# Kernel optimization log

Hardware: AMD Instinct MI355X
Metric: run time of the kernel (lower is better)

Reference implementation:

```python
import jax, jax.numpy as jnp
import numpy as np

N_NODES = 100000
N_EDGES = 1600000
NUM_FEATURES = 64
HIDDEN = 64
NUM_CLASSES = 16


def setup_inputs() -> dict:
    key = jax.random.key(0)
    ks = jax.random.split(key, 8)
    x = jax.random.normal(ks[0], (N_NODES, NUM_FEATURES), dtype=jnp.float32)
    edge_index = jax.random.randint(ks[1], (2, N_EDGES), 0, N_NODES, dtype=jnp.int32)
    # Glorot-ish init for weights, zero bias (matches GCNConv / Linear defaults closely enough)
    s1 = 1.0 / np.sqrt(NUM_FEATURES)
    s2 = 1.0 / np.sqrt(HIDDEN)
    W1 = jax.random.uniform(ks[2], (NUM_FEATURES, HIDDEN), jnp.float32, -s1, s1)
    b1 = jnp.zeros((HIDDEN,), jnp.float32)
    W2 = jax.random.uniform(ks[3], (HIDDEN, HIDDEN), jnp.float32, -s2, s2)
    b2 = jnp.zeros((HIDDEN,), jnp.float32)
    W3 = jax.random.uniform(ks[4], (HIDDEN, NUM_CLASSES), jnp.float32, -s2, s2)
    b3 = jax.random.uniform(ks[5], (NUM_CLASSES,), jnp.float32, -s2, s2)
    return {"x": x, "edge_index": edge_index, "W1": W1, "b1": b1,
            "W2": W2, "b2": b2, "W3": W3, "b3": b3}


def _gcn_layer(x, W, b, src, dst, norm, n_nodes):
    # GCNConv: h = X W; out[i] = sum_{(j->i)} norm_ji * h[j]; out += b
    h = x @ W                                   # [N, H] small dense GEMM
    msg = h[src] * norm[:, None]                # [E+N, H] irregular gather
    out = jax.ops.segment_sum(msg, dst, num_segments=n_nodes)  # scatter-add
    return out + b


def reference(x, edge_index, W1, b1, W2, b2, W3, b3):
    n = x.shape[0]
    loop = jnp.arange(n, dtype=edge_index.dtype)
    # add self-loops (PyG GCNConv default add_self_loops=True)
    src = jnp.concatenate([edge_index[0], loop])
    dst = jnp.concatenate([edge_index[1], loop])
    # symmetric normalization D^{-1/2} A_hat D^{-1/2}
    deg = jax.ops.segment_sum(jnp.ones_like(src, dtype=x.dtype), dst, num_segments=n)
    dis = jax.lax.rsqrt(deg)                    # deg >= 1 due to self-loops
    norm = dis[src] * dis[dst]                  # [E+N]

    h = jax.nn.relu(_gcn_layer(x, W1, b1, src, dst, norm, n))
    # F.dropout(training=False) -> identity (module in eval mode)
    h = jax.nn.relu(_gcn_layer(h, W2, b2, src, dst, norm, n))
    z = h @ W3 + b3
    return jax.nn.log_softmax(z, axis=1), h
```

## Files before the change

kernel.cpp:

```cpp
#include <hip/hip_runtime.h>
#include <hip/hip_bf16.h>

typedef __hip_bfloat16 bf16;
typedef unsigned short ushort;

#define NN 100000
#define NE 1600000
#define NBKT 391
#define BCAP 4608
#define EPB 4096
#define NP1 391
#define NMT 6250

typedef __attribute__((ext_vector_type(8))) short s8v;
typedef __attribute__((ext_vector_type(4))) float f4v;
typedef __attribute__((ext_vector_type(2))) float f2v;

__device__ __forceinline__ float ldf(const void* p, int i, int f32) {
    return f32 ? ((const float*)p)[i] : __bfloat162float(((const bf16*)p)[i]);
}
__device__ __forceinline__ void stf(void* p, int i, int f32, float v) {
    if (f32) ((float*)p)[i] = v;
    else     ((bf16*)p)[i] = __float2bfloat16(v);
}

__device__ __forceinline__ ushort f2b(float f) {
    unsigned u = __builtin_bit_cast(unsigned, f);
    u += 0x7FFF + ((u >> 16) & 1);
    return (ushort)(u >> 16);
}
__device__ __forceinline__ float b2f(ushort h) {
    unsigned u = ((unsigned)h) << 16;
    return __builtin_bit_cast(float, u);
}
__device__ __forceinline__ float blo(unsigned u) {
    return __builtin_bit_cast(float, u << 16);
}
__device__ __forceinline__ float bhi(unsigned u) {
    return __builtin_bit_cast(float, u & 0xffff0000u);
}
__device__ __forceinline__ f2v up2(unsigned u) {
    f2v r; r.x = blo(u); r.y = bhi(u); return r;
}

__global__ void k_sentinel(unsigned* out) {
    if (threadIdx.x == 0 && blockIdx.x == 0) out[0] = 0x461C461Cu;
}

__global__ void k_cnt(const unsigned* __restrict__ x, int* __restrict__ flag,
                      const int* __restrict__ dst, int* __restrict__ cnt) {
    __shared__ int hist[NBKT];
    int b = blockIdx.x, t = threadIdx.x;
    for (int i = t; i < NBKT; i += 256) hist[i] = 0;
    __syncthreads();
    int e0 = b * EPB;
#pragma unroll
    for (int k = 0; k < EPB; k += 256) {
        int e = e0 + k + t;
        if (e < NE) atomicAdd(&hist[dst[e] >> 8], 1);
    }
    __syncthreads();
    for (int i = t; i < NBKT; i += 256) cnt[b * NBKT + i] = hist[i];
    if (b == 0) {
        int c = 0;
        for (int i = t; i < 2048; i += 256) {
            unsigned e7 = (x[i] >> 8) & 0x7F;
            c += (e7 >= 60 && e7 <= 66) ? 1 : 0;
        }
        __syncthreads();
        hist[t] = c;
        __syncthreads();
        for (int s = 128; s > 0; s >>= 1) {
            if (t < s) hist[t] += hist[t + s];
            __syncthreads();
        }
        if (t == 0) *flag = (hist[0] >= 1024) ? 0 : 1;
    }
}

__global__ void k_colscan(const int* __restrict__ cnt, int* __restrict__ prefT,
                          int* __restrict__ btot) {
    __shared__ int s[512];
    int k = blockIdx.x, t = threadIdx.x;
    int v = (t < NP1) ? cnt[t * NBKT + k] : 0;
    s[t] = v;
    __syncthreads();
    for (int d = 1; d < 512; d <<= 1) {
        int add = (t >= d) ? s[t - d] : 0;
        __syncthreads();
        s[t] += add;
        __syncthreads();
    }
    if (t < NP1) prefT[k * NP1 + t] = s[t] - v;
    if (t == 511) btot[k] = s[511];
}

__global__ void k_place(const int* __restrict__ src, const int* __restrict__ dst,
                        const int* __restrict__ prefT, unsigned* __restrict__ bbuf) {
    __shared__ int base[NBKT];
    __shared__ int lcur[NBKT];
    int b = blockIdx.x, t = threadIdx.x;
    for (int i = t; i < NBKT; i += 256) {
        base[i] = prefT[i * NP1 + b];
        lcur[i] = 0;
    }
    __syncthreads();
    int e0 = b * EPB;
#pragma unroll
    for (int k = 0; k < EPB; k += 256) {
        int e = e0 + k + t;
        if (e < NE) {
            int d = dst[e];
            int kb = d >> 8;
            int lp = atomicAdd(&lcur[kb], 1);
            bbuf[kb * BCAP + base[kb] + lp] = ((unsigned)src[e] << 8) | (unsigned)(d & 255);
        }
    }
}

__global__ void k_pass2(const unsigned* __restrict__ bbuf, const int* __restrict__ btot,
                        int* __restrict__ rowptr, float* __restrict__ dis,
                        int* __restrict__ csr_off) {
    __shared__ unsigned vals[BCAP];
    __shared__ int lout[BCAP];
    __shared__ int fh[256], fx[256], fc[256];
    int b = blockIdx.x, t = threadIdx.x;
    int part = 0;
    for (int i = t; i < b; i += 256) part += btot[i];
    fh[t] = part;
    __syncthreads();
    for (int s = 128; s > 0; s >>= 1) {
        if (t < s) fh[t] += fh[t + s];
        __syncthreads();
    }
    int g0 = fh[0];
    int cntb = btot[b];
    if (b == 0 && t == 0) rowptr[NN] = NE;
    __syncthreads();
    const unsigned* in = bbuf + b * BCAP;
    fh[t] = 0;
    __syncthreads();
    for (int i = t; i < cntb; i += 256) {
        unsigned v = in[i];
        vals[i] = v;
        atomicAdd(&fh[v & 255], 1);
    }
    __syncthreads();
    fx[t] = fh[t];
    __syncthreads();
    for (int d = 1; d < 256; d <<= 1) {
        int add = (t >= d) ? fx[t - d] : 0;
        __syncthreads();
        fx[t] += add;
        __syncthreads();
    }
    int n = b * 256 + t;
    int ex = fx[t] - fh[t];
    fc[t] = ex;
    if (n < NN) {
        rowptr[n] = g0 + ex;
        dis[n] = rsqrtf(1.0f + (float)fh[t]);
    }
    __syncthreads();
    for (int i = t; i < cntb; i += 256) {
        unsigned v = vals[i];
        int p = atomicAdd(&fc[v & 255], 1);
        lout[p] = (int)((v >> 8) << 7);
    }
    __syncthreads();
    for (int i = t; i < cntb; i += 256) csr_off[g0 + i] = lout[i];
}

__global__ void __launch_bounds__(256) k_gemm_mfma(
        const void* __restrict__ A, int aBase, const void* __restrict__ W,
        bf16* __restrict__ C, const float* __restrict__ dis,
        const int* __restrict__ flag) {
    int f32 = *flag;
    int t = threadIdx.x;
    if (blockIdx.x == 0 && t < 64) ((ushort*)C)[NN * 64 + t] = 0;
    int lane = t & 63;
    int w = t >> 6;
    int m = lane & 15, q = lane >> 4;

    s8v bh[2][4], bl[2][4];
#pragma unroll
    for (int st = 0; st < 2; st++)
#pragma unroll
        for (int nt = 0; nt < 4; nt++)
#pragma unroll
            for (int j = 0; j < 8; j++) {
                int k = st * 32 + q * 8 + j;
                float wv = ldf(W, k * 64 + nt * 16 + m, f32);
                ushort h = f2b(wv);
                bh[st][nt][j] = (short)h;
                bl[st][nt][j] = (short)f2b(wv - b2f(h));
            }

    ushort* Cu = (ushort*)C;
    int gw = blockIdx.x * 4 + w;
    int nw = gridDim.x * 4;
    for (int mt = gw; mt < NMT; mt += nw) {
        int row = mt * 16 + m;
        s8v ah[2], al[2];
        if (f32) {
            const float* ap = (const float*)A + aBase + row * 64 + q * 8;
#pragma unroll
            for (int st = 0; st < 2; st++) {
                f4v va = *(const f4v*)(ap + st * 32);
                f4v vb = *(const f4v*)(ap + st * 32 + 4);
#pragma unroll
                for (int j = 0; j < 8; j++) {
                    float v = (j < 4) ? va[j] : vb[j - 4];
                    ushort h = f2b(v);
                    ah[st][j] = (short)h;
                    al[st][j] = (short)f2b(v - b2f(h));
                }
            }
        } else {
            const short* ap = (const short*)A + aBase + row * 64 + q * 8;
            ah[0] = *(const s8v*)(ap);
            ah[1] = *(const s8v*)(ap + 32);
        }
        float dr[4];
#pragma unroll
        for (int r = 0; r < 4; r++) dr[r] = dis[mt * 16 + q * 4 + r];
#pragma unroll
        for (int nt = 0; nt < 4; nt++) {
            f4v acc = {0.f, 0.f, 0.f, 0.f};
#pragma unroll
            for (int st = 0; st < 2; st++)
                acc = __builtin_amdgcn_mfma_f32_16x16x32_bf16(ah[st], bh[st][nt], acc, 0, 0, 0);
            if (f32) {
#pragma unroll
                for (int st = 0; st < 2; st++) {
                    acc = __builtin_amdgcn_mfma_f32_16x16x32_bf16(ah[st], bl[st][nt], acc, 0, 0, 0);
                    acc = __builtin_amdgcn_mfma_f32_16x16x32_bf16(al[st], bh[st][nt], acc, 0, 0, 0);
                }
            }
            int col = nt * 16 + m;
#pragma unroll
            for (int r = 0; r < 4; r++) {
                int rr = mt * 16 + q * 4 + r;
                Cu[rr * 64 + col] = f2b(dr[r] * acc[r]);
            }
        }
    }
}

__global__ void __launch_bounds__(256, 8) k_aggregate(
        const bf16* __restrict__ hs, void* hout, int hoBase,
        const float* __restrict__ dis,
        const int* __restrict__ rowptr,
        const int* __restrict__ csr_off,
        const void* __restrict__ bias,
        const int* __restrict__ flag) {
    int f32 = *flag;
    int t = threadIdx.x;
    int l = t & 63;
    int q = l >> 4;
    int m = l & 15;
    int fb = m * 8;
    const char* hb = (const char*)hs;
    float b0 = ldf(bias, m * 4 + 0, f32);
    float b1v = ldf(bias, m * 4 + 1, f32);
    float b2v = ldf(bias, m * 4 + 2, f32);
    float b3v = ldf(bias, m * 4 + 3, f32);
    const int Z = NN * 128;
    int wid = blockIdx.x * 4 + (t >> 6);
    int nwav = gridDim.x * 4;
    for (int n = wid; n < NN; n += nwav) {
        int r0 = rowptr[n], r1 = rowptr[n + 1];
        f2v a01 = {0.f, 0.f}, a23 = {0.f, 0.f};
        int j = r0;
        for (; j + 16 <= r1; j += 16) {
            int o0 = csr_off[j + q];
            int o1 = csr_off[j + 4 + q];
            int o2 = csr_off[j + 8 + q];
            int o3 = csr_off[j + 12 + q];
            uint2 v0 = *(const uint2*)(hb + o0 + fb);
            uint2 v1 = *(const uint2*)(hb + o1 + fb);
            uint2 v2 = *(const uint2*)(hb + o2 + fb);
            uint2 v3 = *(const uint2*)(hb + o3 + fb);
            a01 += up2(v0.x); a23 += up2(v0.y);
            a01 += up2(v1.x); a23 += up2(v1.y);
            a01 += up2(v2.x); a23 += up2(v2.y);
            a01 += up2(v3.x); a23 += up2(v3.y);
        }
        if (j < r1) {
            int i0 = j + q, i1 = j + 4 + q, i2 = j + 8 + q, i3 = j + 12 + q;
            int o0 = csr_off[i0]; o0 = (i0 < r1) ? o0 : Z;
            int o1 = csr_off[i1]; o1 = (i1 < r1) ? o1 : Z;
            int o2 = csr_off[i2]; o2 = (i2 < r1) ? o2 : Z;
            int o3 = csr_off[i3]; o3 = (i3 < r1) ? o3 : Z;
            uint2 v0 = *(const uint2*)(hb + o0 + fb);
            uint2 v1 = *(const uint2*)(hb + o1 + fb);
            uint2 v2 = *(const uint2*)(hb + o2 + fb);
            uint2 v3 = *(const uint2*)(hb + o3 + fb);
            a01 += up2(v0.x); a23 += up2(v0.y);
            a01 += up2(v1.x); a23 += up2(v1.y);
            a01 += up2(v2.x); a23 += up2(v2.y);
            a01 += up2(v3.x); a23 += up2(v3.y);
        }
        float a0 = a01.x, a1 = a01.y, a2 = a23.x, a3 = a23.y;
        a0 += __shfl_xor(a0, 32); a1 += __shfl_xor(a1, 32);
        a2 += __shfl_xor(a2, 32); a3 += __shfl_xor(a3, 32);
        a0 += __shfl_xor(a0, 16); a1 += __shfl_xor(a1, 16);
        a2 += __shfl_xor(a2, 16); a3 += __shfl_xor(a3, 16);
        if (q == 0) {
            uint2 sv = *(const uint2*)(hb + n * 128 + fb);
            float dn = dis[n];
            float o0 = fmaxf(dn * (a0 + blo(sv.x)) + b0, 0.f);
            float o1 = fmaxf(dn * (a1 + bhi(sv.x)) + b1v, 0.f);
            float o2 = fmaxf(dn * (a2 + blo(sv.y)) + b2v, 0.f);
            float o3 = fmaxf(dn * (a3 + bhi(sv.y)) + b3v, 0.f);
            if (f32) {
                float4 ov = {o0, o1, o2, o3};
                *(float4*)((float*)hout + hoBase + n * 64 + m * 4) = ov;
            } else {
                unsigned w0 = (unsigned)f2b(o0) | ((unsigned)f2b(o1) << 16);
                unsigned w1 = (unsigned)f2b(o2) | ((unsigned)f2b(o3) << 16);
                uint2 wv; wv.x = w0; wv.y = w1;
                *(uint2*)((ushort*)hout + hoBase + n * 64 + m * 4) = wv;
            }
        }
    }
}

__global__ void k_head(const void* __restrict__ h2, int hBase,
                       const void* __restrict__ W3, const void* __restrict__ b3,
                       void* out, const int* __restrict__ flag) {
    __shared__ float w[64 * 16];
    __shared__ float hrow[16 * 64];
    int f32 = *flag;
    int t = threadIdx.x;
#pragma unroll
    for (int i = 0; i < 4; i++) w[t + i * 256] = ldf(W3, t + i * 256, f32);
    int r0 = blockIdx.x * 16;
#pragma unroll
    for (int i = 0; i < 4; i++) hrow[t + i * 256] = ldf(h2, hBase + r0 * 64 + t + i * 256, f32);
    __syncthreads();
    int lr = t >> 4, c = t & 15;
    float z = ldf(b3, c, f32);
#pragma unroll
    for (int k = 0; k < 64; k++) z += hrow[lr * 64 + k] * w[k * 16 + c];
    float m = z;
#pragma unroll
    for (int off = 8; off >= 1; off >>= 1) m = fmaxf(m, __shfl_xor(m, off, 16));
    float p = __expf(z - m);
    float s = p;
#pragma unroll
    for (int off = 8; off >= 1; off >>= 1) s += __shfl_xor(s, off, 16);
    stf(out, (r0 + lr) * 16 + c, f32, z - m - __logf(s));
}

extern "C" void kernel_launch(void* const* d_in, const int* in_sizes, int n_in,
                              void* d_out, int out_size, void* d_ws, size_t ws_size,
                              hipStream_t stream) {
    const void* x  = d_in[0];
    const int* ei  = (const int*)d_in[1];
    const void* W1 = d_in[2];
    const void* b1 = d_in[3];
    const void* W2 = d_in[4];
    const void* b2 = d_in[5];
    const void* W3 = d_in[6];
    const void* b3 = d_in[7];

    const size_t NEEDED = (size_t)(1807104 + 3203072) * 4;
    if (ws_size < NEEDED) {
        k_sentinel<<<1, 64, 0, stream>>>((unsigned*)d_out);
        return;
    }
    int*      flag    = (int*)d_ws;
    float*    dis     = (float*)d_ws + 256;
    int*      rowptr  = (int*)d_ws + 102656;
    int*      btot    = (int*)d_ws + 205568;
    int*      csr_off = (int*)d_ws + 207104;
    unsigned* bbuf    = (unsigned*)((int*)d_ws + 1807104);
    int*      cnt     = (int*)d_ws + 1807104 + NBKT * BCAP;
    int*      prefT   = cnt + 153088;
    bf16*     bufA    = (bf16*)bbuf;

    const int* srcp = ei;
    const int* dstp = ei + NE;
    const int HB = NN * 16;

    k_cnt<<<NP1, 256, 0, stream>>>((const unsigned*)x, flag, dstp, cnt);
    k_colscan<<<NBKT, 512, 0, stream>>>(cnt, prefT, btot);
    k_place<<<NP1, 256, 0, stream>>>(srcp, dstp, prefT, bbuf);
    k_pass2<<<NBKT, 256, 0, stream>>>(bbuf, btot, rowptr, dis, csr_off);

    k_gemm_mfma<<<1563, 256, 0, stream>>>(x, 0, W1, bufA, dis, flag);
    k_aggregate<<<2048, 256, 0, stream>>>(bufA, d_out, HB, dis, rowptr,
                                          csr_off, b1, flag);

    k_gemm_mfma<<<1563, 256, 0, stream>>>(d_out, HB, W2, bufA, dis, flag);
    k_aggregate<<<2048, 256, 0, stream>>>(bufA, d_out, HB, dis, rowptr,
                                          csr_off, b2, flag);

    k_head<<<NN / 16, 256, 0, stream>>>(d_out, HB, W3, b3, d_out, flag);
}
```

Measured before the change: 259.4 us.

## Stage bucket placement in shared memory for grouped writes; widen head rows per block

Result: no change. 258.0 us (-0.6%).

```diff
diff --git a/kernel.cpp b/kernel.cpp
--- a/kernel.cpp
+++ b/kernel.cpp
@@ -95,27 +95,62 @@
     if (t == 511) btot[k] = s[511];
 }
 
-__global__ void k_place(const int* __restrict__ src, const int* __restrict__ dst,
-                        const int* __restrict__ prefT, unsigned* __restrict__ bbuf) {
+__global__ void __launch_bounds__(512) k_place(
+        const int* __restrict__ src, const int* __restrict__ dst,
+        const int* __restrict__ prefT, unsigned* __restrict__ bbuf) {
     __shared__ int base[NBKT];
-    __shared__ int lcur[NBKT];
+    __shared__ int hist[NBKT];
+    __shared__ int lofs[512];
+    __shared__ unsigned vals[EPB];
+    __shared__ int addr[EPB];
     int b = blockIdx.x, t = threadIdx.x;
-    for (int i = t; i < NBKT; i += 256) {
+    for (int i = t; i < NBKT; i += 512) {
         base[i] = prefT[i * NP1 + b];
-        lcur[i] = 0;
+        hist[i] = 0;
     }
     __syncthreads();
     int e0 = b * EPB;
-#pragma unroll
-    for (int k = 0; k < EPB; k += 256) {
-        int e = e0 + k + t;
+    unsigned ev[8];
+    int kb[8];
+#pragma unroll
+    for (int k = 0; k < 8; k++) {
+        int e = e0 + k * 512 + t;
         if (e < NE) {
             int d = dst[e];
-            int kb = d >> 8;
-            int lp = atomicAdd(&lcur[kb], 1);
-            bbuf[kb * BCAP + base[kb] + lp] = ((unsigned)src[e] << 8) | (unsigned)(d & 255);
-        }
-    }
+            ev[k] = ((unsigned)src[e] << 8) | (unsigned)(d & 255);
+            kb[k] = d >> 8;
+        } else kb[k] = -1;
+    }
+#pragma unroll
+    for (int k = 0; k < 8; k++)
+        if (kb[k] >= 0) atomicAdd(&hist[kb[k]], 1);
+    __syncthreads();
+    int v = (t < NBKT) ? hist[t] : 0;
+    lofs[t] = v;
+    __syncthreads();
+    for (int d = 1; d < 512; d <<= 1) {
+        int add = (t >= d) ? lofs[t - d] : 0;
+        __syncthreads();
+        lofs[t] += add;
+        __syncthreads();
+    }
+    int ex = lofs[t] - v;
+    __syncthreads();
+    lofs[t] = ex;
+    if (t < NBKT) hist[t] = 0;
+    __syncthreads();
+#pragma unroll
+    for (int k = 0; k < 8; k++) {
+        if (kb[k] >= 0) {
+            int p = atomicAdd(&hist[kb[k]], 1);
+            int li = lofs[kb[k]] + p;
+            vals[li] = ev[k];
+            addr[li] = kb[k] * BCAP + base[kb[k]] + p;
+        }
+    }
+    __syncthreads();
+    int tot = min(EPB, NE - e0);
+    for (int i = t; i < tot; i += 512) bbuf[addr[i]] = vals[i];
 }
 
 __global__ void k_pass2(const unsigned* __restrict__ bbuf, const int* __restrict__ btot,
@@ -330,27 +365,38 @@
                        const void* __restrict__ W3, const void* __restrict__ b3,
                        void* out, const int* __restrict__ flag) {
     __shared__ float w[64 * 16];
-    __shared__ float hrow[16 * 64];
+    __shared__ float hrow[64 * 65];
     int f32 = *flag;
     int t = threadIdx.x;
 #pragma unroll
     for (int i = 0; i < 4; i++) w[t + i * 256] = ldf(W3, t + i * 256, f32);
-    int r0 = blockIdx.x * 16;
-#pragma unroll
-    for (int i = 0; i < 4; i++) hrow[t + i * 256] = ldf(h2, hBase + r0 * 64 + t + i * 256, f32);
+    int r0 = blockIdx.x * 64;
+#pragma unroll
+    for (int i = 0; i < 16; i++) {
+        int idx = t + i * 256;
+        int row = idx >> 6;
+        hrow[row * 65 + (idx & 63)] =
+            (r0 + row < NN) ? ldf(h2, hBase + r0 * 64 + idx, f32) : 0.f;
+    }
     __syncthreads();
     int lr = t >> 4, c = t & 15;
-    float z = ldf(b3, c, f32);
-#pragma unroll
-    for (int k = 0; k < 64; k++) z += hrow[lr * 64 + k] * w[k * 16 + c];
-    float m = z;
-#pragma unroll
-    for (int off = 8; off >= 1; off >>= 1) m = fmaxf(m, __shfl_xor(m, off, 16));
-    float p = __expf(z - m);
-    float s = p;
-#pragma unroll
-    for (int off = 8; off >= 1; off >>= 1) s += __shfl_xor(s, off, 16);
-    stf(out, (r0 + lr) * 16 + c, f32, z - m - __logf(s));
+    float bc = ldf(b3, c, f32);
+#pragma unroll
+    for (int g = 0; g < 4; g++) {
+        int row = lr + g * 16;
+        float z = bc;
+#pragma unroll
+        for (int k = 0; k < 64; k++) z += hrow[row * 65 + k] * w[k * 16 + c];
+        float m = z;
+#pragma unroll
+        for (int off = 8; off >= 1; off >>= 1) m = fmaxf(m, __shfl_xor(m, off, 16));
+        float p = __expf(z - m);
+        float s = p;
+#pragma unroll
+        for (int off = 8; off >= 1; off >>= 1) s += __shfl_xor(s, off, 16);
+        if (r0 + row < NN)
+            stf(out, (r0 + row) * 16 + c, f32, z - m - __logf(s));
+    }
 }
 
 extern "C" void kernel_launch(void* const* d_in, const int* in_sizes, int n_in,
@@ -386,7 +432,7 @@
 
     k_cnt<<<NP1, 256, 0, stream>>>((const unsigned*)x, flag, dstp, cnt);
     k_colscan<<<NBKT, 512, 0, stream>>>(cnt, prefT, btot);
-    k_place<<<NP1, 256, 0, stream>>>(srcp, dstp, prefT, bbuf);
+    k_place<<<NP1, 512, 0, stream>>>(srcp, dstp, prefT, bbuf);
     k_pass2<<<NBKT, 256, 0, stream>>>(bbuf, btot, rowptr, dis, csr_off);
 
     k_gemm_mfma<<<1563, 256, 0, stream>>>(x, 0, W1, bufA, dis, flag);
@@ -397,5 +443,5 @@
     k_aggregate<<<2048, 256, 0, stream>>>(bufA, d_out, HB, dis, rowptr,
                                           csr_off, b2, flag);
 
-    k_head<<<NN / 16, 256, 0, stream>>>(d_out, HB, W3, b3, d_out, flag);
-}
+    k_head<<<1563, 256, 0, stream>>>(d_out, HB, W3, b3, d_out, flag);
+}
```
